# Kernel optimization log

Measured on AMD Instinct MI355X. Metric: run time of the kernel, lower is better.

## Reference

```python
import jax, jax.numpy as jnp
import numpy as np

B, T = 256, 512          # sequences, timesteps (batched over pyro.markov loop)
DATA_DIM = 88            # piano-roll tones
HIDDEN_DIM = 16          # HMM latent states
NN_DIM = 48
NN_CHANNELS = 2
KERNEL = 3


def _uniform(key, shape, fan_in):
    bound = 1.0 / np.sqrt(fan_in)
    return jax.random.uniform(key, shape, minval=-bound, maxval=bound, dtype=jnp.float32)


def setup_inputs() -> dict:
    key = jax.random.key(0)
    ks = jax.random.split(key, 13)
    w = jax.random.randint(ks[0], (B, T, 1), 0, HIDDEN_DIM)
    x = jax.random.randint(ks[1], (B, T, 1), 0, HIDDEN_DIM)
    y = jax.random.uniform(ks[2], (B, T, DATA_DIM), dtype=jnp.float32)
    return {
        "w": w, "x": x, "y": y,
        # nn.Linear(hidden_dim, nn_dim) for x and w one-hots
        "W_xh": _uniform(ks[3], (NN_DIM, HIDDEN_DIM), HIDDEN_DIM),
        "b_xh": _uniform(ks[4], (NN_DIM,), HIDDEN_DIM),
        "W_wh": _uniform(ks[5], (NN_DIM, HIDDEN_DIM), HIDDEN_DIM),
        "b_wh": _uniform(ks[6], (NN_DIM,), HIDDEN_DIM),
        # nn.Linear(nn_channels*data_dim, nn_dim)
        "W_yh": _uniform(ks[7], (NN_DIM, NN_CHANNELS * DATA_DIM), NN_CHANNELS * DATA_DIM),
        "b_yh": _uniform(ks[8], (NN_DIM,), NN_CHANNELS * DATA_DIM),
        # nn.Conv1d(1, nn_channels, 3, padding=1)
        "W_conv": _uniform(ks[9], (NN_CHANNELS, 1, KERNEL), KERNEL),
        "b_conv": _uniform(ks[10], (NN_CHANNELS,), KERNEL),
        # nn.Linear(nn_dim, data_dim)
        "W_hl": _uniform(ks[11], (DATA_DIM, NN_DIM), NN_DIM),
        "b_hl": _uniform(ks[12], (DATA_DIM,), NN_DIM),
    }


def _tones_generator(w, x, y, W_xh, b_xh, W_wh, b_wh, W_yh, b_yh, W_conv, b_conv, W_hl, b_hl):
    b, t, d = y.shape
    # one-hot scatter of the latent state indices (trailing index dim of size 1)
    w_onehot = jax.nn.one_hot(w[..., 0], HIDDEN_DIM, dtype=y.dtype)   # [B,T,H]
    x_onehot = jax.nn.one_hot(x[..., 0], HIDDEN_DIM, dtype=y.dtype)   # [B,T,H]
    # Conv1d(1 -> nn_channels, k=3, pad=1) over the tone axis
    y_nch = y.reshape(b * t, 1, d)                                    # [BT,1,D]
    y_conv = jax.lax.conv_general_dilated(
        y_nch, W_conv, window_strides=(1,), padding=[(1, 1)],
        dimension_numbers=("NCH", "OIH", "NCH"))
    y_conv = jax.nn.relu(y_conv + b_conv[None, :, None])              # [BT,C,D]
    y_conv = y_conv.reshape(b, t, NN_CHANNELS * d)                    # [B,T,C*D]
    h = jax.nn.relu(
        jnp.einsum("bth,nh->btn", x_onehot, W_xh) + b_xh
        + jnp.einsum("bth,nh->btn", w_onehot, W_wh) + b_wh
        + jnp.einsum("btc,nc->btn", y_conv, W_yh) + b_yh)             # [B,T,ND]
    return jnp.einsum("btn,dn->btd", h, W_hl) + b_hl                  # [B,T,D]


def reference(w, x, y, W_xh, b_xh, W_wh, b_wh, W_yh, b_yh, W_conv, b_conv, W_hl, b_hl):
    return _tones_generator(w, x, y, W_xh, b_xh, W_wh, b_wh, W_yh, b_yh,
                            W_conv, b_conv, W_hl, b_hl)
```

## Files before the change

### kernel.cpp

```cpp
#include <hip/hip_runtime.h>
#include <stdint.h>

#define NTOK (256 * 512)
#define TPB 256

typedef short bf16x8 __attribute__((ext_vector_type(8)));
typedef float f32x4 __attribute__((ext_vector_type(4)));
typedef unsigned short u16;
typedef unsigned int u32;

#define B1_U16 10752
#define B2_U16 6144

__device__ __forceinline__ u16 f2bf(float f) {
    u32 u = __float_as_uint(f);
    return (u16)((u + 0x7fffu + ((u >> 16) & 1u)) >> 16);
}
__device__ __forceinline__ u32 cvtpk(float lo, float hi) {
    u32 r;
    asm("v_cvt_pk_bf16_f32 %0, %1, %2" : "=v"(r) : "v"(lo), "v"(hi));
    return r;
}

__global__ __launch_bounds__(256, 1)
void prep_weights(const float* __restrict__ Wxh, const float* __restrict__ bxh,
                  const float* __restrict__ Wwh, const float* __restrict__ bwh,
                  const float* __restrict__ Wyh, const float* __restrict__ byh,
                  const float* __restrict__ Whl, const float* __restrict__ bhl,
                  u16* __restrict__ ws)
{
    int e = blockIdx.x * 256 + threadIdx.x;
    if (e < B1_U16) {
        int j = e & 7, n = (e >> 3) % 48, kc = e / 384;
        int k = kc * 8 + j;
        float v;
        if (k < 176)       v = Wyh[n * 176 + (k & 1) * 88 + (k >> 1)];
        else if (k < 192)  v = Wxh[n * 16 + (k - 176)];
        else if (k < 208)  v = Wwh[n * 16 + (k - 192)];
        else if (k == 208) v = bxh[n] + bwh[n] + byh[n];
        else               v = 0.0f;
        ws[e] = f2bf(v);
    } else if (e < B1_U16 + B2_U16) {
        int e2 = e - B1_U16;
        int j = e2 & 7, dd = (e2 >> 3) % 96, kc = e2 / 768;
        int k = kc * 8 + j;
        float v = 0.0f;
        if (dd < 88) {
            if (k < 48)       v = Whl[dd * 48 + k];
            else if (k == 48) v = bhl[dd];
        }
        ws[e] = f2bf(v);
    }
}

__global__ __launch_bounds__(256, 4)
void tones_v7(const int* __restrict__ widx, const int* __restrict__ xidx,
              const float* __restrict__ y,
              const float* __restrict__ Wconv, const float* __restrict__ bconv,
              const u16* __restrict__ wsb,
              float* __restrict__ out)
{
    __shared__ __align__(16) u16 sH[4 * 1024];

    const int tid = threadIdx.x;
    const int wave = tid >> 6, lane = tid & 63;
    const int q = lane >> 4, c = lane & 15;
    u16* sW = sH + wave * 1024;

    const int tb = blockIdx.x * 64 + wave * 16;
    const float* yc = y + (size_t)(tb + c) * 88;
    const int xv = xidx[tb + c];
    const int wv = widx[tb + c];

    const float wc00 = Wconv[0], wc01 = Wconv[1], wc02 = Wconv[2];
    const float wc10 = Wconv[3], wc11 = Wconv[4], wc12 = Wconv[5];
    const float bc0 = bconv[0], bc1 = bconv[1];

    if (lane < 32) {
        uint4 hz = make_uint4((lane < 16) ? 0x3F80u : 0u, 0, 0, 0);
        *(uint4*)(sW + ((6 + (lane >> 4)) * 16 + (lane & 15)) * 8) = hz;
    }

    f32x4 h0 = {0, 0, 0, 0}, h1 = {0, 0, 0, 0}, h2 = {0, 0, 0, 0};

    const u16* bp1 = wsb + (q * 48 + c) * 8;
    const u16* bp2 = wsb + B1_U16 + (q * 96 + c) * 8;

    bf16x8 gA[3], gB[3];
    gA[0] = *(const bf16x8*)(bp1 + 0 * 8);
    gA[1] = *(const bf16x8*)(bp1 + 16 * 8);
    gA[2] = *(const bf16x8*)(bp1 + 32 * 8);

    #pragma unroll
    for (int ks = 0; ks < 7; ks++) {
        bf16x8* cur = (ks & 1) ? gB : gA;
        bf16x8* nxt = (ks & 1) ? gA : gB;
        if (ks < 6) {
            nxt[0] = *(const bf16x8*)(bp1 + ((ks + 1) * 192 +  0) * 8);
            nxt[1] = *(const bf16x8*)(bp1 + ((ks + 1) * 192 + 16) * 8);
            nxt[2] = *(const bf16x8*)(bp1 + ((ks + 1) * 192 + 32) * 8);
        }
        bf16x8 af;
        if (ks < 5) {
            const int d0 = 16 * ks + 4 * q;
            float p0 = (d0 == 0) ? 0.0f : yc[d0 - 1];
            float4 v4 = *(const float4*)(yc + d0);
            float p5 = yc[d0 + 4];
            float p[6] = {p0, v4.x, v4.y, v4.z, v4.w, p5};
            #pragma unroll
            for (int i = 0; i < 4; i++) {
                float c0 = fmaf(wc00, p[i], fmaf(wc01, p[i + 1], fmaf(wc02, p[i + 2], bc0)));
                float c1 = fmaf(wc10, p[i], fmaf(wc11, p[i + 1], fmaf(wc12, p[i + 2], bc1)));
                u32 pk = cvtpk(fmaxf(c0, 0.0f), fmaxf(c1, 0.0f));
                af[2 * i]     = (short)(pk & 0xFFFF);
                af[2 * i + 1] = (short)(pk >> 16);
            }
        } else if (ks == 5) {
            if (q < 2) {
                const int d0 = 80 + 4 * q;
                float p0 = yc[d0 - 1];
                float4 v4 = *(const float4*)(yc + d0);
                float p5 = (q == 0) ? yc[84] : 0.0f;
                float p[6] = {p0, v4.x, v4.y, v4.z, v4.w, p5};
                #pragma unroll
                for (int i = 0; i < 4; i++) {
                    float c0 = fmaf(wc00, p[i], fmaf(wc01, p[i + 1], fmaf(wc02, p[i + 2], bc0)));
                    float c1 = fmaf(wc10, p[i], fmaf(wc11, p[i + 1], fmaf(wc12, p[i + 2], bc1)));
                    u32 pk = cvtpk(fmaxf(c0, 0.0f), fmaxf(c1, 0.0f));
                    af[2 * i]     = (short)(pk & 0xFFFF);
                    af[2 * i + 1] = (short)(pk >> 16);
                }
            } else {
                const int base = (q - 2) * 8;
                #pragma unroll
                for (int j = 0; j < 8; j++)
                    af[j] = (short)((base + j == xv) ? 0x3F80 : 0);
            }
        } else {
            if (q < 2) {
                const int base = q * 8;
                #pragma unroll
                for (int j = 0; j < 8; j++)
                    af[j] = (short)((base + j == wv) ? 0x3F80 : 0);
            } else {
                #pragma unroll
                for (int j = 0; j < 8; j++)
                    af[j] = (short)((q == 2 && j == 0) ? 0x3F80 : 0);
            }
        }
        h0 = __builtin_amdgcn_mfma_f32_16x16x32_bf16(af, cur[0], h0, 0, 0, 0);
        h1 = __builtin_amdgcn_mfma_f32_16x16x32_bf16(af, cur[1], h1, 0, 0, 0);
        h2 = __builtin_amdgcn_mfma_f32_16x16x32_bf16(af, cur[2], h2, 0, 0, 0);
    }

    bf16x8 b2a[6], b2b[6];
    #pragma unroll
    for (int nt = 0; nt < 6; nt++)
        b2a[nt] = *(const bf16x8*)(bp2 + (nt * 16) * 8);

    #pragma unroll
    for (int r = 0; r < 4; r++) {
        const int row = q * 4 + r;
        sW[((0 + (c >> 3)) * 16 + row) * 8 + (c & 7)] = (u16)cvtpk(fmaxf(h0[r], 0.0f), 0.0f);
        sW[((2 + (c >> 3)) * 16 + row) * 8 + (c & 7)] = (u16)cvtpk(fmaxf(h1[r], 0.0f), 0.0f);
        sW[((4 + (c >> 3)) * 16 + row) * 8 + (c & 7)] = (u16)cvtpk(fmaxf(h2[r], 0.0f), 0.0f);
    }

    #pragma unroll
    for (int nt = 0; nt < 6; nt++)
        b2b[nt] = *(const bf16x8*)(bp2 + (384 + nt * 16) * 8);

    f32x4 o0 = {0,0,0,0}, o1 = {0,0,0,0}, o2 = {0,0,0,0};
    f32x4 o3 = {0,0,0,0}, o4 = {0,0,0,0}, o5 = {0,0,0,0};
    {
        bf16x8 a2 = *(const bf16x8*)(sW + (q * 16 + c) * 8);
        o0 = __builtin_amdgcn_mfma_f32_16x16x32_bf16(a2, b2a[0], o0, 0, 0, 0);
        o1 = __builtin_amdgcn_mfma_f32_16x16x32_bf16(a2, b2a[1], o1, 0, 0, 0);
        o2 = __builtin_amdgcn_mfma_f32_16x16x32_bf16(a2, b2a[2], o2, 0, 0, 0);
        o3 = __builtin_amdgcn_mfma_f32_16x16x32_bf16(a2, b2a[3], o3, 0, 0, 0);
        o4 = __builtin_amdgcn_mfma_f32_16x16x32_bf16(a2, b2a[4], o4, 0, 0, 0);
        o5 = __builtin_amdgcn_mfma_f32_16x16x32_bf16(a2, b2a[5], o5, 0, 0, 0);
    }
    {
        bf16x8 a2 = *(const bf16x8*)(sW + ((4 + q) * 16 + c) * 8);
        o0 = __builtin_amdgcn_mfma_f32_16x16x32_bf16(a2, b2b[0], o0, 0, 0, 0);
        o1 = __builtin_amdgcn_mfma_f32_16x16x32_bf16(a2, b2b[1], o1, 0, 0, 0);
        o2 = __builtin_amdgcn_mfma_f32_16x16x32_bf16(a2, b2b[2], o2, 0, 0, 0);
        o3 = __builtin_amdgcn_mfma_f32_16x16x32_bf16(a2, b2b[3], o3, 0, 0, 0);
        o4 = __builtin_amdgcn_mfma_f32_16x16x32_bf16(a2, b2b[4], o4, 0, 0, 0);
        o5 = __builtin_amdgcn_mfma_f32_16x16x32_bf16(a2, b2b[5], o5, 0, 0, 0);
    }

    float* orow = out + (size_t)(tb + q * 4) * 88;
    #pragma unroll
    for (int r = 0; r < 4; r++) {
        orow[r * 88 +  0 + c] = o0[r];
        orow[r * 88 + 16 + c] = o1[r];
        orow[r * 88 + 32 + c] = o2[r];
        orow[r * 88 + 48 + c] = o3[r];
        orow[r * 88 + 64 + c] = o4[r];
        if (c < 8) orow[r * 88 + 80 + c] = o5[r];
    }
}

extern "C" void kernel_launch(void* const* d_in, const int* in_sizes, int n_in,
                              void* d_out, int out_size, void* d_ws, size_t ws_size,
                              hipStream_t stream) {
    (void)in_sizes; (void)n_in; (void)out_size; (void)ws_size;
    u16* ws = (u16*)d_ws;
    prep_weights<<<dim3(66), dim3(TPB), 0, stream>>>(
        (const float*)d_in[3],  (const float*)d_in[4],
        (const float*)d_in[5],  (const float*)d_in[6],
        (const float*)d_in[7],  (const float*)d_in[8],
        (const float*)d_in[11], (const float*)d_in[12], ws);
    tones_v7<<<dim3(NTOK / 64), dim3(TPB), 0, stream>>>(
        (const int*)d_in[0], (const int*)d_in[1], (const float*)d_in[2],
        (const float*)d_in[9], (const float*)d_in[10], ws, (float*)d_out);
}
```

Before: 136.5 us.

## Stage weights and y tiles into LDS via direct global-to-LDS loads

Each block now copies the full bf16 weight buffer (about 33 KB) and its wave's y rows into shared memory with global_load_lds, then reads MFMA B operands and conv inputs from LDS. Previously every wave fetched weights from global or L2 into registers with double buffering, and y was read with scattered per-lane global loads. The change removes those redundant per-wave global weight fetches and gives coalesced y loads. In exchange LDS use grows to about 63 KB per block, occupancy drops to 2 blocks per CU, and a block-wide barrier is added before compute.

```diff
diff --git a/kernel.cpp b/kernel.cpp
--- a/kernel.cpp
+++ b/kernel.cpp
@@ -11,6 +11,10 @@
 
 #define B1_U16 10752
 #define B2_U16 6144
+#define W_BYTES ((B1_U16 + B2_U16) * 2)
+#define W_CHUNKS (W_BYTES / 16)
+#define YB_U16 2816
+#define H_U16 1024
 
 __device__ __forceinline__ u16 f2bf(float f) {
     u32 u = __float_as_uint(f);
@@ -20,6 +24,16 @@
     u32 r;
     asm("v_cvt_pk_bf16_f32 %0, %1, %2" : "=v"(r) : "v"(lo), "v"(hi));
     return r;
+}
+__device__ __forceinline__ void gll16(const void* g, void* l) {
+    __builtin_amdgcn_global_load_lds(
+        (const __attribute__((address_space(1))) void*)g,
+        (__attribute__((address_space(3))) void*)l, 16, 0, 0);
+}
+__device__ __forceinline__ void gll4(const void* g, void* l) {
+    __builtin_amdgcn_global_load_lds(
+        (const __attribute__((address_space(1))) void*)g,
+        (__attribute__((address_space(3))) void*)l, 4, 0, 0);
 }
 
 __global__ __launch_bounds__(256, 1)
@@ -53,60 +67,73 @@
     }
 }
 
-__global__ __launch_bounds__(256, 4)
-void tones_v7(const int* __restrict__ widx, const int* __restrict__ xidx,
+__global__ __launch_bounds__(256, 2)
+void tones_v8(const int* __restrict__ widx, const int* __restrict__ xidx,
               const float* __restrict__ y,
               const float* __restrict__ Wconv, const float* __restrict__ bconv,
               const u16* __restrict__ wsb,
               float* __restrict__ out)
 {
-    __shared__ __align__(16) u16 sH[4 * 1024];
+    __shared__ __align__(16) u16 lds[32256];
 
     const int tid = threadIdx.x;
     const int wave = tid >> 6, lane = tid & 63;
     const int q = lane >> 4, c = lane & 15;
-    u16* sW = sH + wave * 1024;
 
     const int tb = blockIdx.x * 64 + wave * 16;
-    const float* yc = y + (size_t)(tb + c) * 88;
+
+    #pragma unroll
+    for (int i = 0; i < 8; i++) {
+        const int cb = i * 256 + wave * 64;
+        gll16((const char*)wsb + (cb + lane) * 16, (char*)lds + cb * 16);
+    }
+    if (wave == 0) {
+        const int cb = 2048;
+        gll16((const char*)wsb + (cb + lane) * 16, (char*)lds + cb * 16);
+    }
+
+    u16* sYu = lds + 16896 + wave * YB_U16;
+    {
+        const char* yt = (const char*)(y + (size_t)tb * 88);
+        char* dst = (char*)sYu;
+        #pragma unroll
+        for (int j = 0; j < 5; j++)
+            gll16(yt + j * 1024 + lane * 16, dst + j * 1024);
+        #pragma unroll
+        for (int k = 0; k < 2; k++)
+            gll4(yt + 5120 + k * 256 + lane * 4, dst + 5120 + k * 256);
+    }
+
     const int xv = xidx[tb + c];
     const int wv = widx[tb + c];
-
     const float wc00 = Wconv[0], wc01 = Wconv[1], wc02 = Wconv[2];
     const float wc10 = Wconv[3], wc11 = Wconv[4], wc12 = Wconv[5];
     const float bc0 = bconv[0], bc1 = bconv[1];
 
+    u16* sW = lds + 28160 + wave * H_U16;
     if (lane < 32) {
         uint4 hz = make_uint4((lane < 16) ? 0x3F80u : 0u, 0, 0, 0);
         *(uint4*)(sW + ((6 + (lane >> 4)) * 16 + (lane & 15)) * 8) = hz;
     }
 
+    __syncthreads();
+
+    const float* yr = (const float*)sYu + c * 88;
+
     f32x4 h0 = {0, 0, 0, 0}, h1 = {0, 0, 0, 0}, h2 = {0, 0, 0, 0};
 
-    const u16* bp1 = wsb + (q * 48 + c) * 8;
-    const u16* bp2 = wsb + B1_U16 + (q * 96 + c) * 8;
-
-    bf16x8 gA[3], gB[3];
-    gA[0] = *(const bf16x8*)(bp1 + 0 * 8);
-    gA[1] = *(const bf16x8*)(bp1 + 16 * 8);
-    gA[2] = *(const bf16x8*)(bp1 + 32 * 8);
+    const u16* f1 = lds + (q * 48 + c) * 8;
+    const u16* f2 = lds + B1_U16 + (q * 96 + c) * 8;
 
     #pragma unroll
     for (int ks = 0; ks < 7; ks++) {
-        bf16x8* cur = (ks & 1) ? gB : gA;
-        bf16x8* nxt = (ks & 1) ? gA : gB;
-        if (ks < 6) {
-            nxt[0] = *(const bf16x8*)(bp1 + ((ks + 1) * 192 +  0) * 8);
-            nxt[1] = *(const bf16x8*)(bp1 + ((ks + 1) * 192 + 16) * 8);
-            nxt[2] = *(const bf16x8*)(bp1 + ((ks + 1) * 192 + 32) * 8);
-        }
         bf16x8 af;
         if (ks < 5) {
             const int d0 = 16 * ks + 4 * q;
-            float p0 = (d0 == 0) ? 0.0f : yc[d0 - 1];
-            float4 v4 = *(const float4*)(yc + d0);
-            float p5 = yc[d0 + 4];
-            float p[6] = {p0, v4.x, v4.y, v4.z, v4.w, p5};
+            float p0 = (d0 == 0) ? 0.0f : yr[d0 - 1];
+            f32x4 v4 = *(const f32x4*)(yr + d0);
+            float p5 = yr[d0 + 4];
+            float p[6] = {p0, v4[0], v4[1], v4[2], v4[3], p5};
             #pragma unroll
             for (int i = 0; i < 4; i++) {
                 float c0 = fmaf(wc00, p[i], fmaf(wc01, p[i + 1], fmaf(wc02, p[i + 2], bc0)));
@@ -118,10 +145,10 @@
         } else if (ks == 5) {
             if (q < 2) {
                 const int d0 = 80 + 4 * q;
-                float p0 = yc[d0 - 1];
-                float4 v4 = *(const float4*)(yc + d0);
-                float p5 = (q == 0) ? yc[84] : 0.0f;
-                float p[6] = {p0, v4.x, v4.y, v4.z, v4.w, p5};
+                float p0 = yr[d0 - 1];
+                f32x4 v4 = *(const f32x4*)(yr + d0);
+                float p5 = (q == 0) ? yr[84] : 0.0f;
+                float p[6] = {p0, v4[0], v4[1], v4[2], v4[3], p5};
                 #pragma unroll
                 for (int i = 0; i < 4; i++) {
                     float c0 = fmaf(wc00, p[i], fmaf(wc01, p[i + 1], fmaf(wc02, p[i + 2], bc0)));
@@ -148,15 +175,13 @@
                     af[j] = (short)((q == 2 && j == 0) ? 0x3F80 : 0);
             }
         }
-        h0 = __builtin_amdgcn_mfma_f32_16x16x32_bf16(af, cur[0], h0, 0, 0, 0);
-        h1 = __builtin_amdgcn_mfma_f32_16x16x32_bf16(af, cur[1], h1, 0, 0, 0);
-        h2 = __builtin_amdgcn_mfma_f32_16x16x32_bf16(af, cur[2], h2, 0, 0, 0);
-    }
-
-    bf16x8 b2a[6], b2b[6];
-    #pragma unroll
-    for (int nt = 0; nt < 6; nt++)
-        b2a[nt] = *(const bf16x8*)(bp2 + (nt * 16) * 8);
+        bf16x8 b0 = *(const bf16x8*)(f1 + (ks * 192 +  0) * 8);
+        bf16x8 b1 = *(const bf16x8*)(f1 + (ks * 192 + 16) * 8);
+        bf16x8 b2 = *(const bf16x8*)(f1 + (ks * 192 + 32) * 8);
+        h0 = __builtin_amdgcn_mfma_f32_16x16x32_bf16(af, b0, h0, 0, 0, 0);
+        h1 = __builtin_amdgcn_mfma_f32_16x16x32_bf16(af, b1, h1, 0, 0, 0);
+        h2 = __builtin_amdgcn_mfma_f32_16x16x32_bf16(af, b2, h2, 0, 0, 0);
+    }
 
     #pragma unroll
     for (int r = 0; r < 4; r++) {
@@ -166,29 +191,23 @@
         sW[((4 + (c >> 3)) * 16 + row) * 8 + (c & 7)] = (u16)cvtpk(fmaxf(h2[r], 0.0f), 0.0f);
     }
 
-    #pragma unroll
-    for (int nt = 0; nt < 6; nt++)
-        b2b[nt] = *(const bf16x8*)(bp2 + (384 + nt * 16) * 8);
-
     f32x4 o0 = {0,0,0,0}, o1 = {0,0,0,0}, o2 = {0,0,0,0};
     f32x4 o3 = {0,0,0,0}, o4 = {0,0,0,0}, o5 = {0,0,0,0};
-    {
-        bf16x8 a2 = *(const bf16x8*)(sW + (q * 16 + c) * 8);
-        o0 = __builtin_amdgcn_mfma_f32_16x16x32_bf16(a2, b2a[0], o0, 0, 0, 0);
-        o1 = __builtin_amdgcn_mfma_f32_16x16x32_bf16(a2, b2a[1], o1, 0, 0, 0);
-        o2 = __builtin_amdgcn_mfma_f32_16x16x32_bf16(a2, b2a[2], o2, 0, 0, 0);
-        o3 = __builtin_amdgcn_mfma_f32_16x16x32_bf16(a2, b2a[3], o3, 0, 0, 0);
-        o4 = __builtin_amdgcn_mfma_f32_16x16x32_bf16(a2, b2a[4], o4, 0, 0, 0);
-        o5 = __builtin_amdgcn_mfma_f32_16x16x32_bf16(a2, b2a[5], o5, 0, 0, 0);
-    }
-    {
-        bf16x8 a2 = *(const bf16x8*)(sW + ((4 + q) * 16 + c) * 8);
-        o0 = __builtin_amdgcn_mfma_f32_16x16x32_bf16(a2, b2b[0], o0, 0, 0, 0);
-        o1 = __builtin_amdgcn_mfma_f32_16x16x32_bf16(a2, b2b[1], o1, 0, 0, 0);
-        o2 = __builtin_amdgcn_mfma_f32_16x16x32_bf16(a2, b2b[2], o2, 0, 0, 0);
-        o3 = __builtin_amdgcn_mfma_f32_16x16x32_bf16(a2, b2b[3], o3, 0, 0, 0);
-        o4 = __builtin_amdgcn_mfma_f32_16x16x32_bf16(a2, b2b[4], o4, 0, 0, 0);
-        o5 = __builtin_amdgcn_mfma_f32_16x16x32_bf16(a2, b2b[5], o5, 0, 0, 0);
+    #pragma unroll
+    for (int ks = 0; ks < 2; ks++) {
+        bf16x8 a2 = *(const bf16x8*)(sW + ((ks * 4 + q) * 16 + c) * 8);
+        bf16x8 w0 = *(const bf16x8*)(f2 + (ks * 384 +  0) * 8);
+        bf16x8 w1 = *(const bf16x8*)(f2 + (ks * 384 + 16) * 8);
+        bf16x8 w2 = *(const bf16x8*)(f2 + (ks * 384 + 32) * 8);
+        bf16x8 w3 = *(const bf16x8*)(f2 + (ks * 384 + 48) * 8);
+        bf16x8 w4 = *(const bf16x8*)(f2 + (ks * 384 + 64) * 8);
+        bf16x8 w5 = *(const bf16x8*)(f2 + (ks * 384 + 80) * 8);
+        o0 = __builtin_amdgcn_mfma_f32_16x16x32_bf16(a2, w0, o0, 0, 0, 0);
+        o1 = __builtin_amdgcn_mfma_f32_16x16x32_bf16(a2, w1, o1, 0, 0, 0);
+        o2 = __builtin_amdgcn_mfma_f32_16x16x32_bf16(a2, w2, o2, 0, 0, 0);
+        o3 = __builtin_amdgcn_mfma_f32_16x16x32_bf16(a2, w3, o3, 0, 0, 0);
+        o4 = __builtin_amdgcn_mfma_f32_16x16x32_bf16(a2, w4, o4, 0, 0, 0);
+        o5 = __builtin_amdgcn_mfma_f32_16x16x32_bf16(a2, w5, o5, 0, 0, 0);
     }
 
     float* orow = out + (size_t)(tb + q * 4) * 88;
@@ -213,7 +232,7 @@
         (const float*)d_in[5],  (const float*)d_in[6],
         (const float*)d_in[7],  (const float*)d_in[8],
         (const float*)d_in[11], (const float*)d_in[12], ws);
-    tones_v7<<<dim3(NTOK / 64), dim3(TPB), 0, stream>>>(
+    tones_v8<<<dim3(NTOK / 64), dim3(TPB), 0, stream>>>(
         (const int*)d_in[0], (const int*)d_in[1], (const float*)d_in[2],
         (const float*)d_in[9], (const float*)d_in[10], ws, (float*)d_out);
 }
```

Result: faster. 124.7 us (-8.6%).
